# Kernel tuning notes

Measured on AMD Instinct MI355X. Metric: run time of the kernel, lower is better.

Reference implementation:

```python
import jax, jax.numpy as jnp
import numpy as np

B, T, D, H = 2, 2048, 1024, 16
HD = D // H  # head_dim = 64

def setup_inputs() -> dict:
    key = jax.random.key(0)
    ks = jax.random.split(key, 6)
    s = 1.0 / np.sqrt(D)
    return {
        "x": jax.random.normal(ks[0], (B, T, D), jnp.float32),
        "Wq": jax.random.normal(ks[1], (D, D), jnp.float32) * s,
        "Wk": jax.random.normal(ks[2], (D, D), jnp.float32) * s,
        "Wv": jax.random.normal(ks[3], (D, D), jnp.float32) * s,
        "Wo": jax.random.normal(ks[4], (D, D), jnp.float32) * s,
        "bo": jnp.zeros((D,), jnp.float32),
    }

def reference(x, Wq, Wk, Wv, Wo, bo):
    b, n, _ = x.shape
    # projections -> [b, h, n, hd]
    def split_heads(t):
        return t.reshape(b, n, H, HD).transpose(0, 2, 1, 3)
    q = split_heads(x @ Wq)
    k = split_heads(x @ Wk)
    v = split_heads(x @ Wv)
    scale = HD ** 0.5
    scores = jnp.einsum('bhqd,bhkd->bhqk', q, k) / scale
    causal = jnp.tril(jnp.ones((n, n), bool))  # True = keep
    scores = jnp.where(causal, scores, -jnp.inf)
    attn = jax.nn.softmax(scores, axis=-1)
    ctx = jnp.einsum('bhqk,bhkd->bhqd', attn, v)
    ctx = ctx.transpose(0, 2, 1, 3).reshape(b, n, D)
    return ctx @ Wo + bo
```

## Files before the change

kernel.cpp:

```cpp
#include <hip/hip_runtime.h>
#include <stdint.h>

typedef unsigned short u16;
typedef unsigned int   u32;
typedef __attribute__((ext_vector_type(8))) __bf16 bf8;
typedef __attribute__((ext_vector_type(4))) float  f4;

#define NEG_INF (-__builtin_inff())

#define BB 2
#define TT 2048
#define DD 1024
#define HH 16
#define HD 64
#define BT (BB*TT)

#define SBAR() __builtin_amdgcn_s_barrier()
#define VMCNT4() asm volatile("s_waitcnt vmcnt(4)" ::: "memory")
#define VMCNT0() asm volatile("s_waitcnt vmcnt(0)" ::: "memory")
#define LGKMCNT0() asm volatile("s_waitcnt lgkmcnt(0)" ::: "memory")

__device__ __forceinline__ u16 f2bf(float f) {
  u32 u = __builtin_bit_cast(u32, f);
  u += 0x7FFFu + ((u >> 16) & 1u);
  return (u16)(u >> 16);
}

__device__ __forceinline__ void g2l16(const void* g, void* l) {
  __builtin_amdgcn_global_load_lds((const __attribute__((address_space(1))) u32*)g,
                                   (__attribute__((address_space(3))) u32*)l, 16, 0, 0);
}

__global__ void k_cast_x(const float* __restrict__ x, uint4* __restrict__ xb) {
  int i = blockIdx.x * 256 + threadIdx.x;
  const float4* xf = (const float4*)x;
  float4 a = xf[2*i], b = xf[2*i+1];
  uint4 o;
  o.x = (u32)f2bf(a.x) | ((u32)f2bf(a.y) << 16);
  o.y = (u32)f2bf(a.z) | ((u32)f2bf(a.w) << 16);
  o.z = (u32)f2bf(b.x) | ((u32)f2bf(b.y) << 16);
  o.w = (u32)f2bf(b.z) | ((u32)f2bf(b.w) << 16);
  xb[i] = o;
}

__global__ void k_twcast(const float* __restrict__ w0, const float* __restrict__ w1,
                         const float* __restrict__ w2, const float* __restrict__ w3,
                         u16* __restrict__ o0, u16* __restrict__ o1,
                         u16* __restrict__ o2, u16* __restrict__ o3) {
  const float* W; u16* O;
  switch (blockIdx.z) {
    case 0: W = w0; O = o0; break;
    case 1: W = w1; O = o1; break;
    case 2: W = w2; O = o2; break;
    default: W = w3; O = o3; break;
  }
  __shared__ __align__(16) u16 tile[64][80];
  int tid = threadIdx.x;
  int k0 = blockIdx.y * 64, n0 = blockIdx.x * 64;
#pragma unroll
  for (int it = 0; it < 4; ++it) {
    int c = it*256 + tid; int kr = c >> 4, ns = c & 15;
    float4 v = *(const float4*)(W + (size_t)(k0+kr)*DD + n0 + ns*4);
    u16* p = &tile[kr][ns*4];
    p[0] = f2bf(v.x); p[1] = f2bf(v.y); p[2] = f2bf(v.z); p[3] = f2bf(v.w);
  }
  __syncthreads();
#pragma unroll
  for (int it = 0; it < 2; ++it) {
    int c = it*256 + tid; int nr = c >> 3, ks = c & 7;
    u32 ww[4];
#pragma unroll
    for (int e = 0; e < 4; ++e) {
      u16 lo = tile[ks*8 + 2*e][nr], hi = tile[ks*8 + 2*e + 1][nr];
      ww[e] = (u32)lo | ((u32)hi << 16);
    }
    uint4 o; o.x = ww[0]; o.y = ww[1]; o.z = ww[2]; o.w = ww[3];
    *(uint4*)(O + (size_t)(n0+nr)*DD + k0 + ks*8) = o;
  }
}

__global__ __launch_bounds__(256, 2) void k_qkv(const u16* __restrict__ xb,
    const u16* __restrict__ wqt, const u16* __restrict__ wkt, const u16* __restrict__ wvt,
    u16* __restrict__ qo, u16* __restrict__ ko, u16* __restrict__ vo) {
  __shared__ uint4 smem4[1024];
  char* smem = (char*)smem4;
  int tid = threadIdx.x, w = tid >> 6, l = tid & 63;
  int bid = blockIdx.y * 24 + blockIdx.x;
  int wg = (bid & 7) * 96 + (bid >> 3);
  int nb = wg % 24, mb = wg / 24;
  const u16* Bt = (nb < 8) ? wqt : (nb < 16 ? wkt : wvt);
  int nbl = nb & 7;
  int wm = w >> 1, wn = w & 1;
  f4 z = {0.f, 0.f, 0.f, 0.f};
  f4 acc[4][4];
#pragma unroll
  for (int i = 0; i < 4; ++i)
#pragma unroll
    for (int j = 0; j < 4; ++j) acc[i][j] = z;

  for (int kt = 0; kt < 32; ++kt) {
    int kk = kt * 32;
    __syncthreads();
#pragma unroll
    for (int i = 0; i < 2; ++i) {
      int c = i*256 + tid; int row = c >> 2, u = c & 3, s = u ^ ((row >> 1) & 3);
      g2l16(xb + (size_t)(mb*128 + row)*DD + kk + s*8, smem + (i*256 + w*64)*16);
    }
#pragma unroll
    for (int i = 0; i < 2; ++i) {
      int c = i*256 + tid; int row = c >> 2, u = c & 3, s = u ^ ((row >> 1) & 3);
      g2l16(Bt + (size_t)(nbl*128 + row)*DD + kk + s*8, smem + 8192 + (i*256 + w*64)*16);
    }
    __syncthreads();
    bf8 af[4], bfr[4];
#pragma unroll
    for (int mf = 0; mf < 4; ++mf) {
      int row = wm*64 + mf*16 + (l & 15);
      int s = (l >> 4) ^ ((row >> 1) & 3);
      af[mf] = *(const bf8*)(smem + row*64 + s*16);
    }
#pragma unroll
    for (int nf = 0; nf < 4; ++nf) {
      int row = wn*64 + nf*16 + (l & 15);
      int s = (l >> 4) ^ ((row >> 1) & 3);
      bfr[nf] = *(const bf8*)(smem + 8192 + row*64 + s*16);
    }
#pragma unroll
    for (int mf = 0; mf < 4; ++mf)
#pragma unroll
      for (int nf = 0; nf < 4; ++nf)
        acc[mf][nf] = __builtin_amdgcn_mfma_f32_16x16x32_bf16(af[mf], bfr[nf], acc[mf][nf], 0, 0, 0);
  }
  u16* Out = (nb < 8) ? qo : (nb < 16 ? ko : vo);
#pragma unroll
  for (int mf = 0; mf < 4; ++mf) {
    int m0 = mb*128 + wm*64 + mf*16 + (l >> 4)*4;
    int b = m0 >> 11;
#pragma unroll
    for (int nf = 0; nf < 4; ++nf) {
      int nn = nbl*128 + wn*64 + nf*16 + (l & 15);
      int h = nn >> 6, d = nn & 63;
#pragma unroll
      for (int r = 0; r < 4; ++r) {
        int t = (m0 + r) & 2047;
        Out[(size_t)((b*HH + h)*TT + t)*HD + d] = f2bf(acc[mf][nf][r]);
      }
    }
  }
}

__global__ void k_vt(const u16* __restrict__ v, u16* __restrict__ vt) {
  __shared__ __align__(16) u16 tile[64][80];
  int tid = threadIdx.x;
  int bh = blockIdx.y, t0 = blockIdx.x * 64;
#pragma unroll
  for (int it = 0; it < 2; ++it) {
    int c = it*256 + tid; int tr = c >> 3, ds_ = c & 7;
    uint4 val = *(const uint4*)(v + (size_t)(bh*TT + t0 + tr)*HD + ds_*8);
    *(uint4*)&tile[tr][ds_*8] = val;
  }
  __syncthreads();
#pragma unroll
  for (int it = 0; it < 2; ++it) {
    int c = it*256 + tid; int dr = c >> 3, ts = c & 7;
    u32 ww[4];
#pragma unroll
    for (int e = 0; e < 4; ++e) {
      u16 lo = tile[ts*8 + 2*e][dr], hi = tile[ts*8 + 2*e + 1][dr];
      ww[e] = (u32)lo | ((u32)hi << 16);
    }
    uint4 o; o.x = ww[0]; o.y = ww[1]; o.z = ww[2]; o.w = ww[3];
    *(uint4*)(vt + (size_t)(bh*HD + dr)*TT + t0 + ts*8) = o;
  }
}

__global__ __launch_bounds__(256, 2) void k_attn(const u16* __restrict__ q,
    const u16* __restrict__ kk, const u16* __restrict__ vt, u16* __restrict__ ctx) {
  __shared__ __align__(16) char smem[50176];
  int tid = threadIdx.x, w = tid >> 6, l = tid & 63;
  int fid = blockIdx.x;
  int xcd = fid & 7, j = fid >> 3;
  int bh  = xcd * 4 + (j & 3);
  int ip  = j >> 2;
  char* Pb = smem + 32768 + w * 4352;
  int b = bh >> 4, h = bh & 15;

  auto stageK = [&](int t) {
#pragma unroll
    for (int i = 0; i < 4; ++i) {
      int c = i*256 + tid; int row = c >> 3, u = c & 7;
      g2l16(kk + (size_t)(bh*TT + t*128 + row)*HD + (u ^ (row & 7))*8,
            smem + (i*256 + w*64)*16);
    }
  };
  auto stageV = [&](int t) {
#pragma unroll
    for (int i = 0; i < 4; ++i) {
      int c = i*256 + tid; int row = c >> 4, u = c & 15;
      g2l16(vt + (size_t)(bh*HD + row)*TT + t*128 + (u ^ (row & 15))*8,
            smem + 16384 + (i*256 + w*64)*16);
    }
  };

  for (int ps = 0; ps < 2; ++ps) {
    int q0 = (ps ? (31 - ip) : ip) * 64;
    int qw = q0 + w * 16;
    const u16* qbase = q + (size_t)(bh*TT + qw + (l & 15))*HD + (l >> 4)*8;
    bf8 qf0 = *(const bf8*)(qbase);
    bf8 qf1 = *(const bf8*)(qbase + 32);
    float mreg[4] = {NEG_INF, NEG_INF, NEG_INF, NEG_INF};
    float lreg[4] = {0.f, 0.f, 0.f, 0.f};
    f4 z = {0.f, 0.f, 0.f, 0.f};
    f4 acc[4]; acc[0] = z; acc[1] = z; acc[2] = z; acc[3] = z;
    int nt = (q0 >> 7) + 1;
    stageK(0); stageV(0);
    for (int t = 0; t < nt; ++t) {
      bool last = (t == nt - 1);
      VMCNT4();
      SBAR();
      f4 sv[8];
#pragma unroll
      for (int jf = 0; jf < 8; ++jf) {
        f4 s = z;
        int row = jf*16 + (l & 15);
        int s0 = (l >> 4) ^ (row & 7);
        int s1 = ((l >> 4) + 4) ^ (row & 7);
        bf8 b0 = *(const bf8*)(smem + row*128 + s0*16);
        bf8 b1 = *(const bf8*)(smem + row*128 + s1*16);
        s = __builtin_amdgcn_mfma_f32_16x16x32_bf16(qf0, b0, s, 0, 0, 0);
        s = __builtin_amdgcn_mfma_f32_16x16x32_bf16(qf1, b1, s, 0, 0, 0);
        sv[jf] = s;
      }
      LGKMCNT0();
      SBAR();
      if (!last) stageK(t + 1);
      bool need_mask = (t*128 + 127) > qw;
#pragma unroll
      for (int jf = 0; jf < 8; ++jf) {
        int key = t*128 + jf*16 + (l & 15);
#pragma unroll
        for (int r = 0; r < 4; ++r) {
          float val = sv[jf][r] * 0.125f;
          if (need_mask) {
            int qrow = qw + (l >> 4)*4 + r;
            if (key > qrow) val = NEG_INF;
          }
          sv[jf][r] = val;
        }
      }
      float alpha[4];
#pragma unroll
      for (int r = 0; r < 4; ++r) {
        float mx = sv[0][r];
#pragma unroll
        for (int jf = 1; jf < 8; ++jf) mx = fmaxf(mx, sv[jf][r]);
#pragma unroll
        for (int d = 1; d < 16; d <<= 1) mx = fmaxf(mx, __shfl_xor(mx, d, 64));
        float mnew = fmaxf(mreg[r], mx);
        alpha[r] = __expf(mreg[r] - mnew);
        mreg[r] = mnew;
      }
      float rs[4] = {0.f, 0.f, 0.f, 0.f};
#pragma unroll
      for (int jf = 0; jf < 8; ++jf) {
        int col = jf*16 + (l & 15);
#pragma unroll
        for (int r = 0; r < 4; ++r) {
          float p = __expf(sv[jf][r] - mreg[r]);
          rs[r] += p;
          *(u16*)(Pb + ((l >> 4)*4 + r)*272 + col*2) = f2bf(p);
        }
      }
#pragma unroll
      for (int r = 0; r < 4; ++r) {
        float t_ = rs[r];
#pragma unroll
        for (int d = 1; d < 16; d <<= 1) t_ += __shfl_xor(t_, d, 64);
        lreg[r] = lreg[r]*alpha[r] + t_;
      }
#pragma unroll
      for (int df = 0; df < 4; ++df) {
        f4 a = acc[df];
        a[0] *= alpha[0]; a[1] *= alpha[1]; a[2] *= alpha[2]; a[3] *= alpha[3];
        acc[df] = a;
      }
      if (!last) { VMCNT4(); } else { VMCNT0(); }
      SBAR();
#pragma unroll
      for (int ks = 0; ks < 4; ++ks) {
        bf8 pf = *(const bf8*)(Pb + (l & 15)*272 + ks*64 + (l >> 4)*16);
#pragma unroll
        for (int df = 0; df < 4; ++df) {
          int row = df*16 + (l & 15);
          int sl = (ks*4 + (l >> 4)) ^ (row & 15);
          bf8 vf = *(const bf8*)(smem + 16384 + row*256 + sl*16);
          acc[df] = __builtin_amdgcn_mfma_f32_16x16x32_bf16(pf, vf, acc[df], 0, 0, 0);
        }
      }
      LGKMCNT0();
      SBAR();
      if (!last) stageV(t + 1);
    }
#pragma unroll
    for (int r = 0; r < 4; ++r) {
      float inv = 1.0f / lreg[r];
      int t = q0 + w*16 + (l >> 4)*4 + r;
      u16* dst = ctx + (size_t)(b*TT + t)*DD + h*HD;
#pragma unroll
      for (int df = 0; df < 4; ++df)
        dst[df*16 + (l & 15)] = f2bf(acc[df][r] * inv);
    }
  }
}

__global__ __launch_bounds__(256, 2) void k_out(const u16* __restrict__ ctx,
    const u16* __restrict__ wot, const float* __restrict__ bo, float* __restrict__ out) {
  __shared__ uint4 smem4[1024];
  char* smem = (char*)smem4;
  int tid = threadIdx.x, w = tid >> 6, l = tid & 63;
  int bid = blockIdx.y * 8 + blockIdx.x;
  int wg = (bid & 7) * 32 + (bid >> 3);
  int nb = wg % 8, mb = wg / 8;
  int wm = w >> 1, wn = w & 1;
  f4 z = {0.f, 0.f, 0.f, 0.f};
  f4 acc[4][4];
#pragma unroll
  for (int i = 0; i < 4; ++i)
#pragma unroll
    for (int j = 0; j < 4; ++j) acc[i][j] = z;

  for (int kt = 0; kt < 32; ++kt) {
    int kkk = kt * 32;
    __syncthreads();
#pragma unroll
    for (int i = 0; i < 2; ++i) {
      int c = i*256 + tid; int row = c >> 2, u = c & 3, s = u ^ ((row >> 1) & 3);
      g2l16(ctx + (size_t)(mb*128 + row)*DD + kkk + s*8, smem + (i*256 + w*64)*16);
    }
#pragma unroll
    for (int i = 0; i < 2; ++i) {
      int c = i*256 + tid; int row = c >> 2, u = c & 3, s = u ^ ((row >> 1) & 3);
      g2l16(wot + (size_t)(nb*128 + row)*DD + kkk + s*8, smem + 8192 + (i*256 + w*64)*16);
    }
    __syncthreads();
    bf8 af[4], bfr[4];
#pragma unroll
    for (int mf = 0; mf < 4; ++mf) {
      int row = wm*64 + mf*16 + (l & 15);
      int s = (l >> 4) ^ ((row >> 1) & 3);
      af[mf] = *(const bf8*)(smem + row*64 + s*16);
    }
#pragma unroll
    for (int nf = 0; nf < 4; ++nf) {
      int row = wn*64 + nf*16 + (l & 15);
      int s = (l >> 4) ^ ((row >> 1) & 3);
      bfr[nf] = *(const bf8*)(smem + 8192 + row*64 + s*16);
    }
#pragma unroll
    for (int mf = 0; mf < 4; ++mf)
#pragma unroll
      for (int nf = 0; nf < 4; ++nf)
        acc[mf][nf] = __builtin_amdgcn_mfma_f32_16x16x32_bf16(af[mf], bfr[nf], acc[mf][nf], 0, 0, 0);
  }
#pragma unroll
  for (int nf = 0; nf < 4; ++nf) {
    int n = nb*128 + wn*64 + nf*16 + (l & 15);
    float bias = bo[n];
#pragma unroll
    for (int mf = 0; mf < 4; ++mf) {
      int m0 = mb*128 + wm*64 + mf*16 + (l >> 4)*4;
#pragma unroll
      for (int r = 0; r < 4; ++r)
        out[(size_t)(m0 + r)*DD + n] = acc[mf][nf][r] + bias;
    }
  }
}

extern "C" void kernel_launch(void* const* d_in, const int* in_sizes, int n_in,
                              void* d_out, int out_size, void* d_ws, size_t ws_size,
                              hipStream_t stream) {
  const float* x  = (const float*)d_in[0];
  const float* Wq = (const float*)d_in[1];
  const float* Wk = (const float*)d_in[2];
  const float* Wv = (const float*)d_in[3];
  const float* Wo = (const float*)d_in[4];
  const float* bo = (const float*)d_in[5];
  float* out = (float*)d_out;
  char* ws = (char*)d_ws;

  u16* xb  = (u16*)(ws);
  u16* wqt = (u16*)(ws + 8388608);
  u16* wkt = (u16*)(ws + 10485760);
  u16* wvt = (u16*)(ws + 12582912);
  u16* wot = (u16*)(ws + 14680064);
  u16* qb_ = (u16*)(ws + 16777216);
  u16* kb_ = (u16*)(ws + 25165824);
  u16* vb_ = (u16*)(ws + 33554432);
  u16* vtb = (u16*)(ws + 41943040);
  u16* cxb = (u16*)(ws + 50331648);

  k_cast_x<<<dim3(2048), dim3(256), 0, stream>>>(x, (uint4*)xb);
  k_twcast<<<dim3(16, 16, 4), dim3(256), 0, stream>>>(Wq, Wk, Wv, Wo, wqt, wkt, wvt, wot);
  k_qkv<<<dim3(24, 32), dim3(256), 0, stream>>>(xb, wqt, wkt, wvt, qb_, kb_, vb_);
  k_vt<<<dim3(32, 32), dim3(256), 0, stream>>>(vb_, vtb);
  k_attn<<<dim3(512), dim3(256), 0, stream>>>(qb_, kb_, vtb, cxb);
  k_out<<<dim3(8, 32), dim3(256), 0, stream>>>(cxb, wot, bo, out);
}
```

Before: 200.0 us.

## Fuse V transpose into QKV epilogue and transpose attention MFMA layout

The QKV projection epilogue now writes V directly in transposed [bh, d, t] layout, which removes the separate k_vt kernel launch and its round trip through memory. Q is pre-scaled by log2(e)/sqrt(hd), so attention can use the raw v_exp_f32 (exp2) instead of __expf plus a per-element scale. The MFMA operands are swapped so each lane owns a single query row. That reduces row max and sum to two cross-lane shuffles, lets P be written as packed u32 with an XOR swizzle, and lets the ctx output use 8-byte stores. It also adds s_setprio around the MFMA sections; the risk is correctness of the new layouts and swizzle indexing.

```diff
diff --git a/kernel.cpp b/kernel.cpp
--- a/kernel.cpp
+++ b/kernel.cpp
@@ -24,6 +24,10 @@
   u32 u = __builtin_bit_cast(u32, f);
   u += 0x7FFFu + ((u >> 16) & 1u);
   return (u16)(u >> 16);
+}
+
+__device__ __forceinline__ float exp2fast(float x) {
+  float r; asm("v_exp_f32 %0, %1" : "=v"(r) : "v"(x)); return r;
 }
 
 __device__ __forceinline__ void g2l16(const void* g, void* l) {
@@ -131,46 +135,39 @@
       for (int nf = 0; nf < 4; ++nf)
         acc[mf][nf] = __builtin_amdgcn_mfma_f32_16x16x32_bf16(af[mf], bfr[nf], acc[mf][nf], 0, 0, 0);
   }
-  u16* Out = (nb < 8) ? qo : (nb < 16 ? ko : vo);
-#pragma unroll
-  for (int mf = 0; mf < 4; ++mf) {
-    int m0 = mb*128 + wm*64 + mf*16 + (l >> 4)*4;
-    int b = m0 >> 11;
-#pragma unroll
-    for (int nf = 0; nf < 4; ++nf) {
-      int nn = nbl*128 + wn*64 + nf*16 + (l & 15);
-      int h = nn >> 6, d = nn & 63;
-#pragma unroll
-      for (int r = 0; r < 4; ++r) {
-        int t = (m0 + r) & 2047;
-        Out[(size_t)((b*HH + h)*TT + t)*HD + d] = f2bf(acc[mf][nf][r]);
-      }
-    }
-  }
-}
-
-__global__ void k_vt(const u16* __restrict__ v, u16* __restrict__ vt) {
-  __shared__ __align__(16) u16 tile[64][80];
-  int tid = threadIdx.x;
-  int bh = blockIdx.y, t0 = blockIdx.x * 64;
-#pragma unroll
-  for (int it = 0; it < 2; ++it) {
-    int c = it*256 + tid; int tr = c >> 3, ds_ = c & 7;
-    uint4 val = *(const uint4*)(v + (size_t)(bh*TT + t0 + tr)*HD + ds_*8);
-    *(uint4*)&tile[tr][ds_*8] = val;
-  }
-  __syncthreads();
-#pragma unroll
-  for (int it = 0; it < 2; ++it) {
-    int c = it*256 + tid; int dr = c >> 3, ts = c & 7;
-    u32 ww[4];
-#pragma unroll
-    for (int e = 0; e < 4; ++e) {
-      u16 lo = tile[ts*8 + 2*e][dr], hi = tile[ts*8 + 2*e + 1][dr];
-      ww[e] = (u32)lo | ((u32)hi << 16);
-    }
-    uint4 o; o.x = ww[0]; o.y = ww[1]; o.z = ww[2]; o.w = ww[3];
-    *(uint4*)(vt + (size_t)(bh*HD + dr)*TT + t0 + ts*8) = o;
+  if (nb < 16) {
+    u16* Out = (nb < 8) ? qo : ko;
+    float qs = (nb < 8) ? 0.18033688011112042f : 1.0f;
+#pragma unroll
+    for (int mf = 0; mf < 4; ++mf) {
+      int m0 = mb*128 + wm*64 + mf*16 + (l >> 4)*4;
+      int b = m0 >> 11;
+#pragma unroll
+      for (int nf = 0; nf < 4; ++nf) {
+        int nn = nbl*128 + wn*64 + nf*16 + (l & 15);
+        int h = nn >> 6, d = nn & 63;
+#pragma unroll
+        for (int r = 0; r < 4; ++r) {
+          int t = (m0 + r) & 2047;
+          Out[(size_t)((b*HH + h)*TT + t)*HD + d] = f2bf(acc[mf][nf][r] * qs);
+        }
+      }
+    }
+  } else {
+#pragma unroll
+    for (int mf = 0; mf < 4; ++mf) {
+      int m0 = mb*128 + wm*64 + mf*16 + (l >> 4)*4;
+      int b = m0 >> 11, t0 = m0 & 2047;
+#pragma unroll
+      for (int nf = 0; nf < 4; ++nf) {
+        int nn = nbl*128 + wn*64 + nf*16 + (l & 15);
+        int h = nn >> 6, d = nn & 63;
+        uint2 o;
+        o.x = (u32)f2bf(acc[mf][nf][0]) | ((u32)f2bf(acc[mf][nf][1]) << 16);
+        o.y = (u32)f2bf(acc[mf][nf][2]) | ((u32)f2bf(acc[mf][nf][3]) << 16);
+        *(uint2*)(vo + (size_t)((b*HH + h)*HD + d)*TT + t0) = o;
+      }
+    }
   }
 }
 
@@ -178,12 +175,14 @@
     const u16* __restrict__ kk, const u16* __restrict__ vt, u16* __restrict__ ctx) {
   __shared__ __align__(16) char smem[50176];
   int tid = threadIdx.x, w = tid >> 6, l = tid & 63;
+  int qi = l & 15, g = l >> 4;
   int fid = blockIdx.x;
   int xcd = fid & 7, j = fid >> 3;
   int bh  = xcd * 4 + (j & 3);
   int ip  = j >> 2;
-  char* Pb = smem + 32768 + w * 4352;
+  u32* Pw = (u32*)(smem + 32768) + w * 1088;
   int b = bh >> 4, h = bh & 15;
+  u32 colx = ((u32)(qi & 3)) << 2;
 
   auto stageK = [&](int t) {
 #pragma unroll
@@ -205,11 +204,11 @@
   for (int ps = 0; ps < 2; ++ps) {
     int q0 = (ps ? (31 - ip) : ip) * 64;
     int qw = q0 + w * 16;
-    const u16* qbase = q + (size_t)(bh*TT + qw + (l & 15))*HD + (l >> 4)*8;
+    int qrow = qw + qi;
+    const u16* qbase = q + (size_t)(bh*TT + qrow)*HD + g*8;
     bf8 qf0 = *(const bf8*)(qbase);
     bf8 qf1 = *(const bf8*)(qbase + 32);
-    float mreg[4] = {NEG_INF, NEG_INF, NEG_INF, NEG_INF};
-    float lreg[4] = {0.f, 0.f, 0.f, 0.f};
+    float mreg = NEG_INF, lreg = 0.f;
     f4 z = {0.f, 0.f, 0.f, 0.f};
     f4 acc[4]; acc[0] = z; acc[1] = z; acc[2] = z; acc[3] = z;
     int nt = (q0 >> 7) + 1;
@@ -218,97 +217,90 @@
       bool last = (t == nt - 1);
       VMCNT4();
       SBAR();
+      __builtin_amdgcn_s_setprio(1);
       f4 sv[8];
 #pragma unroll
       for (int jf = 0; jf < 8; ++jf) {
         f4 s = z;
-        int row = jf*16 + (l & 15);
-        int s0 = (l >> 4) ^ (row & 7);
-        int s1 = ((l >> 4) + 4) ^ (row & 7);
+        int row = jf*16 + qi;
+        int s0 = g ^ (row & 7);
+        int s1 = (g + 4) ^ (row & 7);
         bf8 b0 = *(const bf8*)(smem + row*128 + s0*16);
         bf8 b1 = *(const bf8*)(smem + row*128 + s1*16);
-        s = __builtin_amdgcn_mfma_f32_16x16x32_bf16(qf0, b0, s, 0, 0, 0);
-        s = __builtin_amdgcn_mfma_f32_16x16x32_bf16(qf1, b1, s, 0, 0, 0);
+        s = __builtin_amdgcn_mfma_f32_16x16x32_bf16(b0, qf0, s, 0, 0, 0);
+        s = __builtin_amdgcn_mfma_f32_16x16x32_bf16(b1, qf1, s, 0, 0, 0);
         sv[jf] = s;
       }
+      __builtin_amdgcn_s_setprio(0);
       LGKMCNT0();
       SBAR();
       if (!last) stageK(t + 1);
-      bool need_mask = (t*128 + 127) > qw;
+      if (t*128 + 127 > qw) {
+        int cbase = qrow - t*128 - 4*g;
+#pragma unroll
+        for (int jf = 0; jf < 8; ++jf)
+#pragma unroll
+          for (int r = 0; r < 4; ++r)
+            if (jf*16 + r > cbase) sv[jf][r] = NEG_INF;
+      }
+      float mx = NEG_INF;
+#pragma unroll
+      for (int jf = 0; jf < 8; ++jf)
+        mx = fmaxf(mx, fmaxf(fmaxf(sv[jf][0], sv[jf][1]), fmaxf(sv[jf][2], sv[jf][3])));
+      mx = fmaxf(mx, __shfl_xor(mx, 16, 64));
+      mx = fmaxf(mx, __shfl_xor(mx, 32, 64));
+      float mnew = fmaxf(mreg, mx);
+      float alpha = exp2fast(mreg - mnew);
+      mreg = mnew;
+      float rs = 0.f;
 #pragma unroll
       for (int jf = 0; jf < 8; ++jf) {
-        int key = t*128 + jf*16 + (l & 15);
-#pragma unroll
-        for (int r = 0; r < 4; ++r) {
-          float val = sv[jf][r] * 0.125f;
-          if (need_mask) {
-            int qrow = qw + (l >> 4)*4 + r;
-            if (key > qrow) val = NEG_INF;
-          }
-          sv[jf][r] = val;
-        }
-      }
-      float alpha[4];
-#pragma unroll
-      for (int r = 0; r < 4; ++r) {
-        float mx = sv[0][r];
-#pragma unroll
-        for (int jf = 1; jf < 8; ++jf) mx = fmaxf(mx, sv[jf][r]);
-#pragma unroll
-        for (int d = 1; d < 16; d <<= 1) mx = fmaxf(mx, __shfl_xor(mx, d, 64));
-        float mnew = fmaxf(mreg[r], mx);
-        alpha[r] = __expf(mreg[r] - mnew);
-        mreg[r] = mnew;
-      }
-      float rs[4] = {0.f, 0.f, 0.f, 0.f};
-#pragma unroll
-      for (int jf = 0; jf < 8; ++jf) {
-        int col = jf*16 + (l & 15);
-#pragma unroll
-        for (int r = 0; r < 4; ++r) {
-          float p = __expf(sv[jf][r] - mreg[r]);
-          rs[r] += p;
-          *(u16*)(Pb + ((l >> 4)*4 + r)*272 + col*2) = f2bf(p);
-        }
-      }
-#pragma unroll
-      for (int r = 0; r < 4; ++r) {
-        float t_ = rs[r];
-#pragma unroll
-        for (int d = 1; d < 16; d <<= 1) t_ += __shfl_xor(t_, d, 64);
-        lreg[r] = lreg[r]*alpha[r] + t_;
-      }
+        float p0 = exp2fast(sv[jf][0] - mreg);
+        float p1 = exp2fast(sv[jf][1] - mreg);
+        float p2 = exp2fast(sv[jf][2] - mreg);
+        float p3 = exp2fast(sv[jf][3] - mreg);
+        rs += (p0 + p1) + (p2 + p3);
+        u32 pk0 = (u32)f2bf(p0) | ((u32)f2bf(p1) << 16);
+        u32 pk1 = (u32)f2bf(p2) | ((u32)f2bf(p3) << 16);
+        Pw[qi*68 + ((u32)(jf*8 + 2*g + 0) ^ colx)] = pk0;
+        Pw[qi*68 + ((u32)(jf*8 + 2*g + 1) ^ colx)] = pk1;
+      }
+      rs += __shfl_xor(rs, 16, 64);
+      rs += __shfl_xor(rs, 32, 64);
+      lreg = lreg * alpha + rs;
 #pragma unroll
       for (int df = 0; df < 4; ++df) {
         f4 a = acc[df];
-        a[0] *= alpha[0]; a[1] *= alpha[1]; a[2] *= alpha[2]; a[3] *= alpha[3];
+        a[0] *= alpha; a[1] *= alpha; a[2] *= alpha; a[3] *= alpha;
         acc[df] = a;
       }
       if (!last) { VMCNT4(); } else { VMCNT0(); }
       SBAR();
+      __builtin_amdgcn_s_setprio(1);
 #pragma unroll
       for (int ks = 0; ks < 4; ++ks) {
-        bf8 pf = *(const bf8*)(Pb + (l & 15)*272 + ks*64 + (l >> 4)*16);
+        bf8 pf = *(const bf8*)(Pw + qi*68 + ((u32)(ks*16 + 4*g) ^ colx));
 #pragma unroll
         for (int df = 0; df < 4; ++df) {
-          int row = df*16 + (l & 15);
-          int sl = (ks*4 + (l >> 4)) ^ (row & 15);
+          int row = df*16 + qi;
+          int sl = (ks*4 + g) ^ (row & 15);
           bf8 vf = *(const bf8*)(smem + 16384 + row*256 + sl*16);
-          acc[df] = __builtin_amdgcn_mfma_f32_16x16x32_bf16(pf, vf, acc[df], 0, 0, 0);
+          acc[df] = __builtin_amdgcn_mfma_f32_16x16x32_bf16(vf, pf, acc[df], 0, 0, 0);
         }
       }
+      __builtin_amdgcn_s_setprio(0);
       LGKMCNT0();
       SBAR();
       if (!last) stageV(t + 1);
     }
-#pragma unroll
-    for (int r = 0; r < 4; ++r) {
-      float inv = 1.0f / lreg[r];
-      int t = q0 + w*16 + (l >> 4)*4 + r;
-      u16* dst = ctx + (size_t)(b*TT + t)*DD + h*HD;
-#pragma unroll
-      for (int df = 0; df < 4; ++df)
-        dst[df*16 + (l & 15)] = f2bf(acc[df][r] * inv);
+    float inv = 1.0f / lreg;
+    u16* dst = ctx + (size_t)(b*TT + qrow)*DD + h*HD;
+#pragma unroll
+    for (int df = 0; df < 4; ++df) {
+      uint2 o;
+      o.x = (u32)f2bf(acc[df][0] * inv) | ((u32)f2bf(acc[df][1] * inv) << 16);
+      o.y = (u32)f2bf(acc[df][2] * inv) | ((u32)f2bf(acc[df][3] * inv) << 16);
+      *(uint2*)(dst + df*16 + 4*g) = o;
     }
   }
 }
@@ -395,14 +387,12 @@
   u16* wot = (u16*)(ws + 14680064);
   u16* qb_ = (u16*)(ws + 16777216);
   u16* kb_ = (u16*)(ws + 25165824);
-  u16* vb_ = (u16*)(ws + 33554432);
   u16* vtb = (u16*)(ws + 41943040);
   u16* cxb = (u16*)(ws + 50331648);
 
   k_cast_x<<<dim3(2048), dim3(256), 0, stream>>>(x, (uint4*)xb);
   k_twcast<<<dim3(16, 16, 4), dim3(256), 0, stream>>>(Wq, Wk, Wv, Wo, wqt, wkt, wvt, wot);
-  k_qkv<<<dim3(24, 32), dim3(256), 0, stream>>>(xb, wqt, wkt, wvt, qb_, kb_, vb_);
-  k_vt<<<dim3(32, 32), dim3(256), 0, stream>>>(vb_, vtb);
+  k_qkv<<<dim3(24, 32), dim3(256), 0, stream>>>(xb, wqt, wkt, wvt, qb_, kb_, vtb);
   k_attn<<<dim3(512), dim3(256), 0, stream>>>(qb_, kb_, vtb, cxb);
   k_out<<<dim3(8, 32), dim3(256), 0, stream>>>(cxb, wot, bo, out);
 }
```

After: 184.8 us. 7.6% less time.
